# Optimization experiments

Measured on AMD Instinct MI355X. Metric: run time of the kernel, lower is better.

## Reference

```python
import jax, jax.numpy as jnp
import numpy as np

B, S, H = 2, 2048, 2048
V = 32000
NSEG, R, TM = 16, 256, 1024  # num_segments, rank, math seq len (== N_max)
BETA1, BETA2, BETA3 = 0.5, 0.5, 0.4


def setup_inputs() -> dict:
    key = jax.random.key(0)
    ks = jax.random.split(key, 8)
    last_hidden_state = jax.random.normal(ks[0], (B, S, H), dtype=jnp.float32)
    input_ids = jax.random.randint(ks[1], (B, S), 0, V)
    attention_mask = jnp.ones((B, S), dtype=jnp.int32)
    starts = jax.random.randint(ks[2], (B,), 0, 512)
    ends = starts + 512 + jax.random.randint(ks[3], (B,), 0, 512)  # starts < ends < S-1
    math_labels = jax.random.randint(ks[4], (B, TM), 0, V)
    math_attention_mask = jnp.ones((B, TM), dtype=jnp.int32)
    math_lengths = jnp.full((B,), TM, dtype=jnp.int64)
    # parameters (xavier-uniform-like for A/B, small normal for lm_head)
    lim_a = np.sqrt(6.0 / (H + R)).astype(np.float32)
    A_matrices = jax.random.uniform(ks[5], (NSEG, H, R), minval=-lim_a, maxval=lim_a, dtype=jnp.float32)
    B_matrices = jax.random.uniform(ks[6], (NSEG, R, H), minval=-lim_a, maxval=lim_a, dtype=jnp.float32)
    bias = jnp.zeros((NSEG, H), dtype=jnp.float32)
    W = jax.random.normal(ks[7], (V, H), dtype=jnp.float32) * 0.02
    return {"last_hidden_state": last_hidden_state, "input_ids": input_ids,
            "attention_mask": attention_mask, "starts": starts, "ends": ends,
            "math_labels": math_labels, "math_attention_mask": math_attention_mask,
            "math_lengths": math_lengths, "A_matrices": A_matrices,
            "B_matrices": B_matrices, "bias": bias, "W": W}


def _masked_mean(loss, mask):
    m = mask.astype(loss.dtype)
    return jnp.sum(loss * m) / jnp.maximum(jnp.sum(m), 1.0)


def _nll(logits, labels):
    logp = jax.nn.log_softmax(logits, axis=-1)
    return -jnp.take_along_axis(logp, labels[..., None], axis=-1)[..., 0]


def reference(last_hidden_state, input_ids, attention_mask, starts, ends,
              math_labels, math_attention_mask, math_lengths,
              A_matrices, B_matrices, bias, W):
    # ---- simple-talk / final-answer loss on full-sequence lm_head logits ----
    logits = jnp.einsum('bsh,vh->bsv', last_hidden_state, W)            # [B,S,V]
    nll = _nll(logits[:, :-1, :], input_ids[:, 1:])                     # [B,S-1]
    idx = jnp.arange(S - 1)[None, :]
    real_len = jnp.sum(attention_mask, axis=1, keepdims=True)
    mask_st = (idx >= starts[:, None] - 1) & (idx <= ends[:, None] - 1)
    mask_fa = (idx >= ends[:, None]) & (idx < real_len - 1)
    simple_talk_loss = _masked_mean(nll, mask_st)
    final_answer_loss = _masked_mean(nll, mask_fa)
    # ---- math loss: segment-routed low-rank adapter (grouped GEMM form) ----
    # token at math position p uses segment p // ceil(N_max/NSEG); with TM==N_max
    # segments are contiguous chunks, so reshape [B,TM,H] -> [B,NSEG,chunk,H].
    chunk = TM // NSEG
    pos = starts[:, None] + jnp.arange(TM)[None, :]                     # [B,TM]
    xm = jnp.take_along_axis(last_hidden_state, pos[:, :, None], axis=1)
    x = xm.reshape(B, NSEG, chunk, H)
    inter = jnp.einsum('bsch,srh->bscr', x, B_matrices)                 # B @ h
    trans = jnp.einsum('bscr,shr->bsch', inter, A_matrices) + bias[None, :, None, :]
    mlogits = jnp.einsum('bsch,vh->bscv', trans, W)                     # [B,NSEG,chunk,V]
    mnll = _nll(mlogits, math_labels.reshape(B, NSEG, chunk))
    math_loss = _masked_mean(mnll, math_attention_mask.reshape(B, NSEG, chunk))
    total_loss = BETA1 * math_loss + BETA2 * simple_talk_loss + BETA3 * final_answer_loss
    return total_loss, math_loss, simple_talk_loss, final_answer_loss
```

## Files before the change

### kernel.cpp

```cpp
#include <hip/hip_runtime.h>

typedef __bf16 bf16x8 __attribute__((ext_vector_type(8)));
typedef float f32x4 __attribute__((ext_vector_type(4)));
typedef float f32x2 __attribute__((ext_vector_type(2)));
typedef int i32x4 __attribute__((ext_vector_type(4)));
typedef int i32x2 __attribute__((ext_vector_type(2)));
typedef int i32x8 __attribute__((ext_vector_type(8)));

#define B_ 2
#define S_ 2048
#define H_ 2048
#define V_ 32000
#define NSEG_ 16
#define R_ 256
#define TM_ 1024
#define MAIN_ROWS 4096
#define MROWS 6144

#define WSCALE 512.0f
#define WSCALE_INV 0.001953125f

__device__ __forceinline__ unsigned short f2bf(float f) {
  union { float f; unsigned u; } v; v.f = f;
  unsigned r = (v.u + 0x7fffu + ((v.u >> 16) & 1u)) >> 16;
  return (unsigned short)r;
}

__device__ __forceinline__ i32x4 pack8(const float* __restrict__ src) {
  float4 v0 = *(const float4*)src;
  float4 v1 = *(const float4*)(src + 4);
  union { unsigned short u[8]; i32x4 v; } o;
  o.u[0] = f2bf(v0.x); o.u[1] = f2bf(v0.y); o.u[2] = f2bf(v0.z); o.u[3] = f2bf(v0.w);
  o.u[4] = f2bf(v1.x); o.u[5] = f2bf(v1.y); o.u[6] = f2bf(v1.z); o.u[7] = f2bf(v1.w);
  return o.v;
}

__device__ __forceinline__ unsigned e4m3_enc(float f) {
  unsigned u = __float_as_uint(f);
  unsigned s = (u >> 24) & 0x80u;
  float a = fabsf(f);
  unsigned mag;
  if (a >= 0.015625f) {
    unsigned b = __float_as_uint(a);
    b += 0x7FFFFu + ((b >> 20) & 1u);
    int e = (int)(b >> 23) - 120;
    unsigned m = (b >> 20) & 7u;
    if (e > 15) { e = 15; m = 6; }
    mag = ((unsigned)e << 3) | m;
  } else {
    mag = (unsigned)__float2int_rn(a * 512.f);
  }
  return s | mag;
}

__device__ __forceinline__ float e4m3_dec(unsigned b) {
  unsigned e = (b >> 3) & 15u, m = b & 7u;
  float mag = e ? __uint_as_float(((e + 120u) << 23) | (m << 20))
                : (float)m * 0.001953125f;
  return (b & 0x80u) ? -mag : mag;
}

__device__ __forceinline__ int pk_fp8x4(float a, float b, float c, float d) {
#if __has_builtin(__builtin_amdgcn_cvt_pk_fp8_f32)
  int w = __builtin_amdgcn_cvt_pk_fp8_f32(a, b, 0, false);
  w = __builtin_amdgcn_cvt_pk_fp8_f32(c, d, w, true);
  return w;
#else
  return (int)e4m3_enc(a) | ((int)e4m3_enc(b) << 8) |
         ((int)e4m3_enc(c) << 16) | ((int)e4m3_enc(d) << 24);
#endif
}

__device__ __forceinline__ unsigned char fp8_1(float v) {
#if __has_builtin(__builtin_amdgcn_cvt_pk_fp8_f32)
  int w = __builtin_amdgcn_cvt_pk_fp8_f32(v, 0.f, 0, false);
  return (unsigned char)(w & 0xff);
#else
  return (unsigned char)e4m3_enc(v);
#endif
}

__device__ __forceinline__ void fp8x4_dec(int v, float* o) {
#if __has_builtin(__builtin_amdgcn_cvt_pk_f32_fp8)
  f32x2 lo = __builtin_amdgcn_cvt_pk_f32_fp8(v, false);
  f32x2 hi = __builtin_amdgcn_cvt_pk_f32_fp8(v, true);
  o[0] = lo[0]; o[1] = lo[1]; o[2] = hi[0]; o[3] = hi[1];
#else
  o[0] = e4m3_dec(v & 0xff); o[1] = e4m3_dec((v >> 8) & 0xff);
  o[2] = e4m3_dec((v >> 16) & 0xff); o[3] = e4m3_dec((v >> 24) & 0xff);
#endif
}

__global__ void quant_fp8_k(const float* __restrict__ in, int* __restrict__ out,
                            float scale, int n16) {
  int i = blockIdx.x * 256 + threadIdx.x;
  if (i >= n16) return;
  const float4* p = (const float4*)in + (size_t)i * 4;
  float4 v0 = p[0], v1 = p[1], v2 = p[2], v3 = p[3];
  i32x4 o;
  o[0] = pk_fp8x4(v0.x * scale, v0.y * scale, v0.z * scale, v0.w * scale);
  o[1] = pk_fp8x4(v1.x * scale, v1.y * scale, v1.z * scale, v1.w * scale);
  o[2] = pk_fp8x4(v2.x * scale, v2.y * scale, v2.z * scale, v2.w * scale);
  o[3] = pk_fp8x4(v3.x * scale, v3.y * scale, v3.z * scale, v3.w * scale);
  *((i32x4*)out + i) = o;
}

__global__ __launch_bounds__(256)
void adapter1_k(const float* __restrict__ lhs, const int* __restrict__ starts,
                const float* __restrict__ Bm, unsigned short* __restrict__ interb) {
  const int g = blockIdx.x;
  const int b = g >> 4, seg = g & 15;
  __shared__ __align__(16) unsigned short At[64 * 72];
  __shared__ __align__(16) unsigned short Bt[256 * 72];
  const int tid = threadIdx.x;
  const int wave = tid >> 6, lane = tid & 63;
  const int quad = lane >> 4, l16 = lane & 15;
  const int start = starts[b];

  f32x4 acc[4][4];
  for (int i = 0; i < 4; ++i)
    for (int j = 0; j < 4; ++j)
      acc[i][j] = (f32x4){0.f, 0.f, 0.f, 0.f};

  for (int k0 = 0; k0 < H_; k0 += 64) {
    for (int i = 0; i < 2; ++i) {
      int c = tid + i * 256;
      int row = c >> 3, p = c & 7;
      int t = seg * 64 + row;
      const float* src = lhs + ((size_t)b * S_ + start + t) * H_ + k0 + p * 8;
      *(i32x4*)(&At[row * 72 + p * 8]) = pack8(src);
    }
    for (int i = 0; i < 8; ++i) {
      int c = tid + i * 256;
      int row = c >> 3, p = c & 7;
      const float* src = Bm + ((size_t)seg * R_ + row) * H_ + k0 + p * 8;
      *(i32x4*)(&Bt[row * 72 + p * 8]) = pack8(src);
    }
    __syncthreads();
    for (int kk = 0; kk < 64; kk += 32) {
      bf16x8 af[4], bfr[4];
      for (int rt = 0; rt < 4; ++rt)
        af[rt] = __builtin_bit_cast(bf16x8,
            *(const i32x4*)(&At[(rt * 16 + l16) * 72 + kk + quad * 8]));
      for (int ct = 0; ct < 4; ++ct)
        bfr[ct] = __builtin_bit_cast(bf16x8,
            *(const i32x4*)(&Bt[(wave * 64 + ct * 16 + l16) * 72 + kk + quad * 8]));
      for (int rt = 0; rt < 4; ++rt)
        for (int ct = 0; ct < 4; ++ct)
          acc[rt][ct] = __builtin_amdgcn_mfma_f32_16x16x32_bf16(
              af[rt], bfr[ct], acc[rt][ct], 0, 0, 0);
    }
    __syncthreads();
  }
  for (int rt = 0; rt < 4; ++rt)
    for (int ct = 0; ct < 4; ++ct)
      for (int r = 0; r < 4; ++r) {
        int m = rt * 16 + quad * 4 + r;
        int n = wave * 64 + ct * 16 + l16;
        interb[((size_t)g * 64 + m) * R_ + n] = f2bf(acc[rt][ct][r]);
      }
}

__global__ __launch_bounds__(256)
void adapter2_k(const unsigned short* __restrict__ interb, const float* __restrict__ Am,
                const float* __restrict__ bias, unsigned char* __restrict__ Xq) {
  const int g = blockIdx.x >> 3;
  const int nt = blockIdx.x & 7;
  const int seg = g & 15;
  __shared__ __align__(16) unsigned short At[64 * 72];
  __shared__ __align__(16) unsigned short Bt[256 * 72];
  const int tid = threadIdx.x;
  const int wave = tid >> 6, lane = tid & 63;
  const int quad = lane >> 4, l16 = lane & 15;

  f32x4 acc[4][4];
  for (int i = 0; i < 4; ++i)
    for (int j = 0; j < 4; ++j)
      acc[i][j] = (f32x4){0.f, 0.f, 0.f, 0.f};

  for (int k0 = 0; k0 < R_; k0 += 64) {
    for (int i = 0; i < 2; ++i) {
      int c = tid + i * 256;
      int row = c >> 3, p = c & 7;
      *(i32x4*)(&At[row * 72 + p * 8]) =
          *(const i32x4*)(interb + ((size_t)g * 64 + row) * R_ + k0 + p * 8);
    }
    for (int i = 0; i < 8; ++i) {
      int c = tid + i * 256;
      int row = c >> 3, p = c & 7;
      const float* src = Am + ((size_t)seg * H_ + nt * 256 + row) * R_ + k0 + p * 8;
      *(i32x4*)(&Bt[row * 72 + p * 8]) = pack8(src);
    }
    __syncthreads();
    for (int kk = 0; kk < 64; kk += 32) {
      bf16x8 af[4], bfr[4];
      for (int rt = 0; rt < 4; ++rt)
        af[rt] = __builtin_bit_cast(bf16x8,
            *(const i32x4*)(&At[(rt * 16 + l16) * 72 + kk + quad * 8]));
      for (int ct = 0; ct < 4; ++ct)
        bfr[ct] = __builtin_bit_cast(bf16x8,
            *(const i32x4*)(&Bt[(wave * 64 + ct * 16 + l16) * 72 + kk + quad * 8]));
      for (int rt = 0; rt < 4; ++rt)
        for (int ct = 0; ct < 4; ++ct)
          acc[rt][ct] = __builtin_amdgcn_mfma_f32_16x16x32_bf16(
              af[rt], bfr[ct], acc[rt][ct], 0, 0, 0);
    }
    __syncthreads();
  }
  for (int rt = 0; rt < 4; ++rt)
    for (int ct = 0; ct < 4; ++ct)
      for (int r = 0; r < 4; ++r) {
        int m = rt * 16 + quad * 4 + r;
        int h = nt * 256 + wave * 64 + ct * 16 + l16;
        float v = acc[rt][ct][r] + bias[seg * H_ + h];
        Xq[((size_t)(MAIN_ROWS + g * 64 + m)) * H_ + h] = fp8_1(v);
      }
}

#define BM 128
#define BN 128
#define BKB 128

__global__ __launch_bounds__(256)
void ce_gemm_k(const unsigned char* __restrict__ X, const unsigned char* __restrict__ Wq,
               const int* __restrict__ starts, float* __restrict__ rowsum) {
  const int m0 = blockIdx.x * BM;
  const int n0 = blockIdx.y * BN;
  if (m0 < MAIN_ROWS) {
    int b = m0 >> 11;
    if (m0 + BM - 1 < starts[b] - 1) return;
  }
  __shared__ __align__(16) unsigned char At[BM * BKB];
  __shared__ __align__(16) unsigned char Bt[BN * BKB];
  const int tid = threadIdx.x;
  const int wave = tid >> 6, lane = tid & 63;
  const int quad = lane >> 4, l16 = lane & 15;
  const int wrow = (wave >> 1) * 64, wcol = (wave & 1) * 64;

  const int rsub = lane >> 3;
  const int clog = (lane & 7) ^ rsub;
  const unsigned char* ag = X  + (size_t)(m0 + 32 * wave + rsub) * H_ + clog * 16;
  const unsigned char* bg = Wq + (size_t)(n0 + 32 * wave + rsub) * H_ + clog * 16;
  unsigned char* al = &At[(32 * wave) * BKB];
  unsigned char* bl = &Bt[(32 * wave) * BKB];

  f32x4 acc[4][4];
  for (int i = 0; i < 4; ++i)
    for (int j = 0; j < 4; ++j)
      acc[i][j] = (f32x4){0.f, 0.f, 0.f, 0.f};

  const int r7 = l16 & 7;
  const int p0 = (2 * quad) ^ r7;
  const int p1 = (2 * quad + 1) ^ r7;

  for (int k0 = 0; k0 < H_; k0 += BKB) {
    #pragma unroll
    for (int j = 0; j < 4; ++j) {
      __builtin_amdgcn_global_load_lds(
          (const __attribute__((address_space(1))) void*)(ag + (size_t)(8 * j) * H_ + k0),
          (__attribute__((address_space(3))) void*)(al + 8 * j * BKB), 16, 0, 0);
      __builtin_amdgcn_global_load_lds(
          (const __attribute__((address_space(1))) void*)(bg + (size_t)(8 * j) * H_ + k0),
          (__attribute__((address_space(3))) void*)(bl + 8 * j * BKB), 16, 0, 0);
    }
    __syncthreads();
    i32x8 af[4], bfr[4];
    #pragma unroll
    for (int rt = 0; rt < 4; ++rt) {
      const unsigned char* base = &At[(wrow + rt * 16 + l16) * BKB];
      i32x4 lo = *(const i32x4*)(base + p0 * 16);
      i32x4 hi = *(const i32x4*)(base + p1 * 16);
      i32x8 t;
      t[0] = lo[0]; t[1] = lo[1]; t[2] = lo[2]; t[3] = lo[3];
      t[4] = hi[0]; t[5] = hi[1]; t[6] = hi[2]; t[7] = hi[3];
      af[rt] = t;
    }
    #pragma unroll
    for (int ct = 0; ct < 4; ++ct) {
      const unsigned char* base = &Bt[(wcol + ct * 16 + l16) * BKB];
      i32x4 lo = *(const i32x4*)(base + p0 * 16);
      i32x4 hi = *(const i32x4*)(base + p1 * 16);
      i32x8 t;
      t[0] = lo[0]; t[1] = lo[1]; t[2] = lo[2]; t[3] = lo[3];
      t[4] = hi[0]; t[5] = hi[1]; t[6] = hi[2]; t[7] = hi[3];
      bfr[ct] = t;
    }
    #pragma unroll
    for (int rt = 0; rt < 4; ++rt)
      #pragma unroll
      for (int ct = 0; ct < 4; ++ct)
        acc[rt][ct] = __builtin_amdgcn_mfma_scale_f32_16x16x128_f8f6f4(
            af[rt], bfr[ct], acc[rt][ct],
            0 , 0 , 0, 127 , 0, 118 );
    __syncthreads();
  }

  for (int rt = 0; rt < 4; ++rt) {
    float s[4] = {0.f, 0.f, 0.f, 0.f};
    for (int ct = 0; ct < 4; ++ct)
      for (int r = 0; r < 4; ++r)
        s[r] += __expf(acc[rt][ct][r]);
    for (int m = 1; m < 16; m <<= 1)
      for (int r = 0; r < 4; ++r)
        s[r] += __shfl_xor(s[r], m, 64);
    if (l16 == 0) {
      for (int r = 0; r < 4; ++r) {
        int grow = m0 + wrow + rt * 16 + quad * 4 + r;
        atomicAdd(&rowsum[grow], s[r]);
      }
    }
  }
}

__global__ void tlogit_k(const unsigned char* __restrict__ Xq,
                         const unsigned char* __restrict__ Wq,
                         const int* __restrict__ input_ids,
                         const int* __restrict__ mlabels,
                         float* __restrict__ tlog) {
  int i = blockIdx.x;
  int label;
  if (i < MAIN_ROWS) {
    int b = i >> 11, s = i & 2047;
    label = (s < S_ - 1) ? input_ids[b * S_ + s + 1] : 0;
  } else {
    int j = i - MAIN_ROWS;
    int b = j >> 10, t = j & 1023;
    label = mlabels[b * TM_ + t];
  }
  const unsigned char* x = Xq + (size_t)i * H_;
  const unsigned char* w = Wq + (size_t)label * H_;
  int tid = threadIdx.x;
  i32x2 xv = *(const i32x2*)(x + tid * 8);
  i32x2 wv = *(const i32x2*)(w + tid * 8);
  float acc = 0.f;
  for (int q = 0; q < 2; ++q) {
    float xf[4], wf[4];
    fp8x4_dec(xv[q], xf);
    fp8x4_dec(wv[q], wf);
    acc += xf[0] * wf[0] + xf[1] * wf[1] + xf[2] * wf[2] + xf[3] * wf[3];
  }
  for (int m = 1; m < 64; m <<= 1) acc += __shfl_xor(acc, m, 64);
  __shared__ float red[4];
  if ((tid & 63) == 0) red[tid >> 6] = acc;
  __syncthreads();
  if (tid == 0) tlog[i] = (red[0] + red[1] + red[2] + red[3]) * WSCALE_INV;
}

__global__ void finalize_k(const float* __restrict__ rowsum, const float* __restrict__ tlog,
                           const int* __restrict__ attn, const int* __restrict__ starts,
                           const int* __restrict__ ends, const int* __restrict__ mmask,
                           float* __restrict__ out) {
  int tid = threadIdx.x;
  __shared__ int tmp[8];
  __shared__ float red[24];
  int s0 = 0, s1 = 0;
  for (int s = tid; s < S_; s += 256) { s0 += attn[s]; s1 += attn[S_ + s]; }
  for (int m = 1; m < 64; m <<= 1) { s0 += __shfl_xor(s0, m, 64); s1 += __shfl_xor(s1, m, 64); }
  if ((tid & 63) == 0) { tmp[(tid >> 6) * 2] = s0; tmp[(tid >> 6) * 2 + 1] = s1; }
  __syncthreads();
  int rl[2];
  rl[0] = tmp[0] + tmp[2] + tmp[4] + tmp[6];
  rl[1] = tmp[1] + tmp[3] + tmp[5] + tmp[7];

  float st_s = 0.f, st_c = 0.f, fa_s = 0.f, fa_c = 0.f, m_s = 0.f, m_c = 0.f;
  for (int i = tid; i < MAIN_ROWS; i += 256) {
    int b = i >> 11, s = i & 2047;
    if (s < S_ - 1) {
      bool stm = (s >= starts[b] - 1) && (s <= ends[b] - 1);
      bool fam = (s >= ends[b]) && (s < rl[b] - 1);
      if (stm || fam) {
        float nll = logf(rowsum[i]) - tlog[i];
        if (stm) { st_s += nll; st_c += 1.f; }
        if (fam) { fa_s += nll; fa_c += 1.f; }
      }
    }
  }
  for (int i = tid; i < B_ * TM_; i += 256) {
    int row = MAIN_ROWS + i;
    float nll = logf(rowsum[row]) - tlog[row];
    float m = (float)mmask[i];
    m_s += nll * m; m_c += m;
  }
  float vals[6] = {st_s, st_c, fa_s, fa_c, m_s, m_c};
  for (int m = 1; m < 64; m <<= 1)
    for (int q = 0; q < 6; ++q) vals[q] += __shfl_xor(vals[q], m, 64);
  if ((tid & 63) == 0)
    for (int q = 0; q < 6; ++q) red[(tid >> 6) * 6 + q] = vals[q];
  __syncthreads();
  if (tid == 0) {
    float stS = red[0] + red[6] + red[12] + red[18];
    float stC = red[1] + red[7] + red[13] + red[19];
    float faS = red[2] + red[8] + red[14] + red[20];
    float faC = red[3] + red[9] + red[15] + red[21];
    float mS  = red[4] + red[10] + red[16] + red[22];
    float mC  = red[5] + red[11] + red[17] + red[23];
    float st = stS / fmaxf(stC, 1.f);
    float fa = faS / fmaxf(faC, 1.f);
    float ml = mS / fmaxf(mC, 1.f);
    out[0] = 0.5f * ml + 0.5f * st + 0.4f * fa;
    out[1] = ml;
    out[2] = st;
    out[3] = fa;
  }
}

extern "C" void kernel_launch(void* const* d_in, const int* in_sizes, int n_in,
                              void* d_out, int out_size, void* d_ws, size_t ws_size,
                              hipStream_t stream) {
  (void)in_sizes; (void)n_in; (void)out_size; (void)ws_size;
  const float* lhs      = (const float*)d_in[0];
  const int* input_ids  = (const int*)d_in[1];
  const int* attn       = (const int*)d_in[2];
  const int* starts     = (const int*)d_in[3];
  const int* ends       = (const int*)d_in[4];
  const int* mlabels    = (const int*)d_in[5];
  const int* mmask      = (const int*)d_in[6];
  const float* Am       = (const float*)d_in[8];
  const float* Bm       = (const float*)d_in[9];
  const float* bias     = (const float*)d_in[10];
  const float* Wf       = (const float*)d_in[11];
  float* out = (float*)d_out;

  char* ws = (char*)d_ws;
  unsigned char* Wq     = (unsigned char*)ws;
  unsigned char* Xq     = (unsigned char*)(ws + 65536000);
  unsigned short* interb= (unsigned short*)(ws + 78118912);
  float* rowsum         = (float*)(ws + 79167488);
  float* tlog           = (float*)(ws + 79192064);

  hipMemsetAsync(rowsum, 0, MROWS * sizeof(float), stream);
  quant_fp8_k<<<(V_ * H_ / 16 + 255) / 256, 256, 0, stream>>>(Wf, (int*)Wq, WSCALE, V_ * H_ / 16);
  quant_fp8_k<<<(MAIN_ROWS * H_ / 16 + 255) / 256, 256, 0, stream>>>(lhs, (int*)Xq, 1.0f, MAIN_ROWS * H_ / 16);
  adapter1_k<<<B_ * NSEG_, 256, 0, stream>>>(lhs, starts, Bm, interb);
  adapter2_k<<<B_ * NSEG_ * 8, 256, 0, stream>>>(interb, Am, bias, Xq);
  ce_gemm_k<<<dim3(MROWS / BM, V_ / BN), 256, 0, stream>>>(Xq, Wq, starts, rowsum);
  tlogit_k<<<MROWS, 256, 0, stream>>>(Xq, Wq, input_ids, mlabels, tlog);
  finalize_k<<<1, 256, 0, stream>>>(rowsum, tlog, attn, starts, ends, mmask, out);
}
```

Before: 1.040 ms.

## Enlarge CE GEMM tile to 256x256 with double-buffered async LDS prefetch

Grows the fp8 cross-entropy GEMM block tile from 128x128 to 256x256 and runs it with 8 waves instead of 4. The K loop is double-buffered: global_load_lds prefetches for the next K tiles are interleaved between quadrant MFMA groups, with explicit vmcnt/lgkmcnt waits, barriers and s_setprio around the MFMAs. The goal is to hide global-memory latency behind compute and get more reuse from each loaded tile. The 128KB of LDS per block limits occupancy to one block per CU, and the hand-written wait counts add risk to correctness and the schedule.

```diff
diff --git a/kernel.cpp b/kernel.cpp
--- a/kernel.cpp
+++ b/kernel.cpp
@@ -217,11 +217,57 @@
       }
 }
 
-#define BM 128
-#define BN 128
+#define BM 256
+#define BN 256
 #define BKB 128
-
-__global__ __launch_bounds__(256)
+#define NKT (H_ / BKB)
+
+#define STAGE_A(kt, h) { \
+  _Pragma("unroll") \
+  for (int j = 0; j < 2; ++j) \
+    __builtin_amdgcn_global_load_lds( \
+        (const __attribute__((address_space(1))) void*)(ag + (size_t)((h) * 128 + j * 64) * H_ + (size_t)(kt) * BKB), \
+        (__attribute__((address_space(3))) void*)(&Abuf[(kt) & 1][((h) * 128 + j * 64 + wave * 8) * BKB]), 16, 0, 0); }
+
+#define STAGE_B(kt, h) { \
+  _Pragma("unroll") \
+  for (int j = 0; j < 2; ++j) \
+    __builtin_amdgcn_global_load_lds( \
+        (const __attribute__((address_space(1))) void*)(bg + (size_t)((h) * 128 + j * 64) * H_ + (size_t)(kt) * BKB), \
+        (__attribute__((address_space(3))) void*)(&Bbuf[(kt) & 1][((h) * 128 + j * 64 + wave * 8) * BKB]), 16, 0, 0); }
+
+#define READ_A(bufi, hrt) { \
+  _Pragma("unroll") \
+  for (int rt = 0; rt < 4; ++rt) { \
+    const unsigned char* base_ = &Abuf[bufi][(wm * 128 + (hrt) * 64 + rt * 16 + l16) * BKB]; \
+    i32x4 lo_ = *(const i32x4*)(base_ + cp0 * 16); \
+    i32x4 hi_ = *(const i32x4*)(base_ + (cp0 ^ 1) * 16); \
+    i32x8 t_; \
+    t_[0] = lo_[0]; t_[1] = lo_[1]; t_[2] = lo_[2]; t_[3] = lo_[3]; \
+    t_[4] = hi_[0]; t_[5] = hi_[1]; t_[6] = hi_[2]; t_[7] = hi_[3]; \
+    af[rt] = t_; } }
+
+#define READ_B(bufi, qc) { \
+  _Pragma("unroll") \
+  for (int ct = 0; ct < 2; ++ct) { \
+    const unsigned char* base_ = &Bbuf[bufi][(wn * 64 + (qc) * 32 + ct * 16 + l16) * BKB]; \
+    i32x4 lo_ = *(const i32x4*)(base_ + cp0 * 16); \
+    i32x4 hi_ = *(const i32x4*)(base_ + (cp0 ^ 1) * 16); \
+    i32x8 t_; \
+    t_[0] = lo_[0]; t_[1] = lo_[1]; t_[2] = lo_[2]; t_[3] = lo_[3]; \
+    t_[4] = hi_[0]; t_[5] = hi_[1]; t_[6] = hi_[2]; t_[7] = hi_[3]; \
+    bf[(qc) * 2 + ct] = t_; } }
+
+#define MFMA_Q(rbase, cbase) { \
+  _Pragma("unroll") \
+  for (int rt = 0; rt < 4; ++rt) \
+    _Pragma("unroll") \
+    for (int ct = 0; ct < 2; ++ct) \
+      acc[(rbase) + rt][(cbase) + ct] = __builtin_amdgcn_mfma_scale_f32_16x16x128_f8f6f4( \
+          af[rt], bf[(cbase) + ct], acc[(rbase) + rt][(cbase) + ct], \
+          0 , 0 , 0, 127 , 0, 118 ); }
+
+__global__ __launch_bounds__(512, 2)
 void ce_gemm_k(const unsigned char* __restrict__ X, const unsigned char* __restrict__ Wq,
                const int* __restrict__ starts, float* __restrict__ rowsum) {
   const int m0 = blockIdx.x * BM;
@@ -230,82 +276,91 @@
     int b = m0 >> 11;
     if (m0 + BM - 1 < starts[b] - 1) return;
   }
-  __shared__ __align__(16) unsigned char At[BM * BKB];
-  __shared__ __align__(16) unsigned char Bt[BN * BKB];
+  __shared__ __align__(16) unsigned char Abuf[2][BM * BKB];
+  __shared__ __align__(16) unsigned char Bbuf[2][BN * BKB];
   const int tid = threadIdx.x;
   const int wave = tid >> 6, lane = tid & 63;
   const int quad = lane >> 4, l16 = lane & 15;
-  const int wrow = (wave >> 1) * 64, wcol = (wave & 1) * 64;
+  const int wm = wave >> 2, wn = wave & 3;
 
   const int rsub = lane >> 3;
   const int clog = (lane & 7) ^ rsub;
-  const unsigned char* ag = X  + (size_t)(m0 + 32 * wave + rsub) * H_ + clog * 16;
-  const unsigned char* bg = Wq + (size_t)(n0 + 32 * wave + rsub) * H_ + clog * 16;
-  unsigned char* al = &At[(32 * wave) * BKB];
-  unsigned char* bl = &Bt[(32 * wave) * BKB];
-
-  f32x4 acc[4][4];
-  for (int i = 0; i < 4; ++i)
+  const unsigned char* ag = X  + (size_t)(m0 + wave * 8 + rsub) * H_ + clog * 16;
+  const unsigned char* bg = Wq + (size_t)(n0 + wave * 8 + rsub) * H_ + clog * 16;
+
+  const int cp0 = (2 * quad) ^ (l16 & 7);
+
+  f32x4 acc[8][4];
+  #pragma unroll
+  for (int i = 0; i < 8; ++i)
+    #pragma unroll
     for (int j = 0; j < 4; ++j)
       acc[i][j] = (f32x4){0.f, 0.f, 0.f, 0.f};
 
-  const int r7 = l16 & 7;
-  const int p0 = (2 * quad) ^ r7;
-  const int p1 = (2 * quad + 1) ^ r7;
-
-  for (int k0 = 0; k0 < H_; k0 += BKB) {
+  i32x8 af[4], bf[4];
+
+  STAGE_B(0, 0); STAGE_B(0, 1);
+  STAGE_A(0, 0); STAGE_A(0, 1);
+  STAGE_B(1, 0); STAGE_B(1, 1);
+  asm volatile("s_waitcnt vmcnt(4)" ::: "memory");
+  __builtin_amdgcn_s_barrier();
+
+  for (int kt = 0; kt < NKT; ++kt) {
+    const int bufi = kt & 1;
+    READ_A(bufi, 0);
+    READ_B(bufi, 0);
+    if (kt + 1 < NKT) STAGE_A(kt + 1, 0);
+    __builtin_amdgcn_s_barrier();
+    asm volatile("s_waitcnt lgkmcnt(0)" ::: "memory");
+    __builtin_amdgcn_s_setprio(1);
+    MFMA_Q(0, 0);
+    __builtin_amdgcn_s_setprio(0);
+    __builtin_amdgcn_s_barrier();
+    READ_B(bufi, 1);
+    if (kt + 1 < NKT) STAGE_A(kt + 1, 1);
+    __builtin_amdgcn_s_barrier();
+    asm volatile("s_waitcnt lgkmcnt(0)" ::: "memory");
+    __builtin_amdgcn_s_setprio(1);
+    MFMA_Q(0, 2);
+    __builtin_amdgcn_s_setprio(0);
+    __builtin_amdgcn_s_barrier();
+    READ_A(bufi, 1);
+    if (kt + 2 < NKT) STAGE_B(kt + 2, 0);
+    __builtin_amdgcn_s_barrier();
+    asm volatile("s_waitcnt lgkmcnt(0)" ::: "memory");
+    __builtin_amdgcn_s_setprio(1);
+    MFMA_Q(4, 0);
+    __builtin_amdgcn_s_setprio(0);
+    __builtin_amdgcn_s_barrier();
+    if (kt + 2 < NKT) STAGE_B(kt + 2, 1);
+    __builtin_amdgcn_s_barrier();
+    __builtin_amdgcn_s_setprio(1);
+    MFMA_Q(4, 2);
+    __builtin_amdgcn_s_setprio(0);
+    if (kt < NKT - 2)
+      asm volatile("s_waitcnt vmcnt(4)" ::: "memory");
+    else
+      asm volatile("s_waitcnt vmcnt(0)" ::: "memory");
+    __builtin_amdgcn_s_barrier();
+  }
+
+  #pragma unroll
+  for (int rt = 0; rt < 8; ++rt) {
+    float s[4] = {0.f, 0.f, 0.f, 0.f};
     #pragma unroll
-    for (int j = 0; j < 4; ++j) {
-      __builtin_amdgcn_global_load_lds(
-          (const __attribute__((address_space(1))) void*)(ag + (size_t)(8 * j) * H_ + k0),
-          (__attribute__((address_space(3))) void*)(al + 8 * j * BKB), 16, 0, 0);
-      __builtin_amdgcn_global_load_lds(
-          (const __attribute__((address_space(1))) void*)(bg + (size_t)(8 * j) * H_ + k0),
-          (__attribute__((address_space(3))) void*)(bl + 8 * j * BKB), 16, 0, 0);
-    }
-    __syncthreads();
-    i32x8 af[4], bfr[4];
-    #pragma unroll
-    for (int rt = 0; rt < 4; ++rt) {
-      const unsigned char* base = &At[(wrow + rt * 16 + l16) * BKB];
-      i32x4 lo = *(const i32x4*)(base + p0 * 16);
-      i32x4 hi = *(const i32x4*)(base + p1 * 16);
-      i32x8 t;
-      t[0] = lo[0]; t[1] = lo[1]; t[2] = lo[2]; t[3] = lo[3];
-      t[4] = hi[0]; t[5] = hi[1]; t[6] = hi[2]; t[7] = hi[3];
-      af[rt] = t;
-    }
-    #pragma unroll
-    for (int ct = 0; ct < 4; ++ct) {
-      const unsigned char* base = &Bt[(wcol + ct * 16 + l16) * BKB];
-      i32x4 lo = *(const i32x4*)(base + p0 * 16);
-      i32x4 hi = *(const i32x4*)(base + p1 * 16);
-      i32x8 t;
-      t[0] = lo[0]; t[1] = lo[1]; t[2] = lo[2]; t[3] = lo[3];
-      t[4] = hi[0]; t[5] = hi[1]; t[6] = hi[2]; t[7] = hi[3];
-      bfr[ct] = t;
-    }
-    #pragma unroll
-    for (int rt = 0; rt < 4; ++rt)
+    for (int ct = 0; ct < 4; ++ct)
       #pragma unroll
-      for (int ct = 0; ct < 4; ++ct)
-        acc[rt][ct] = __builtin_amdgcn_mfma_scale_f32_16x16x128_f8f6f4(
-            af[rt], bfr[ct], acc[rt][ct],
-            0 , 0 , 0, 127 , 0, 118 );
-    __syncthreads();
-  }
-
-  for (int rt = 0; rt < 4; ++rt) {
-    float s[4] = {0.f, 0.f, 0.f, 0.f};
-    for (int ct = 0; ct < 4; ++ct)
       for (int r = 0; r < 4; ++r)
         s[r] += __expf(acc[rt][ct][r]);
+    #pragma unroll
     for (int m = 1; m < 16; m <<= 1)
+      #pragma unroll
       for (int r = 0; r < 4; ++r)
         s[r] += __shfl_xor(s[r], m, 64);
     if (l16 == 0) {
+      #pragma unroll
       for (int r = 0; r < 4; ++r) {
-        int grow = m0 + wrow + rt * 16 + quad * 4 + r;
+        int grow = m0 + wm * 128 + rt * 16 + quad * 4 + r;
         atomicAdd(&rowsum[grow], s[r]);
       }
     }
@@ -433,7 +488,7 @@
   quant_fp8_k<<<(MAIN_ROWS * H_ / 16 + 255) / 256, 256, 0, stream>>>(lhs, (int*)Xq, 1.0f, MAIN_ROWS * H_ / 16);
   adapter1_k<<<B_ * NSEG_, 256, 0, stream>>>(lhs, starts, Bm, interb);
   adapter2_k<<<B_ * NSEG_ * 8, 256, 0, stream>>>(interb, Am, bias, Xq);
-  ce_gemm_k<<<dim3(MROWS / BM, V_ / BN), 256, 0, stream>>>(Xq, Wq, starts, rowsum);
+  ce_gemm_k<<<dim3(MROWS / BM, V_ / BN), 512, 0, stream>>>(Xq, Wq, starts, rowsum);
   tlogit_k<<<MROWS, 256, 0, stream>>>(Xq, Wq, input_ids, mlabels, tlog);
   finalize_k<<<1, 256, 0, stream>>>(rowsum, tlog, attn, starts, ends, mmask, out);
 }
```

Result: slower. 1.154 ms (+11.0%).
